# Performance work log

Hardware: AMD Instinct MI355X
Metric: run time of the kernel (lower is better)

Reference implementation:

```python
import jax, jax.numpy as jnp
import numpy as np

B, P, C = 2, 512, 21          # images, proposals/image, classes (incl background)
REG = 5                       # xc, yc, w, h, angle(deg)
DET = 100                     # detections_per_img
IMW, IMH = 1024, 800
SCORE_THRESH = 0.05
NMS_THR = 0.5
WEIGHTS = (10.0, 10.0, 5.0, 5.0, 3.0)
BBOX_XFORM_CLIP = float(np.log(1000.0 / 16.0))
MAXV = 8                      # max vertices of quad-quad intersection


def setup_inputs() -> dict:
    key = jax.random.key(0)
    k1, k2, k3 = jax.random.split(key, 3)
    class_logits = jax.random.normal(k1, (B * P, C), jnp.float32)
    box_regression = jax.random.normal(k2, (B * P, C * REG), jnp.float32)
    u = jax.random.uniform(k3, (B * P, 5), jnp.float32)
    rrects = jnp.stack([
        u[:, 0] * IMW,            # xc
        u[:, 1] * IMH,            # yc
        u[:, 2] * 200.0 + 16.0,   # w
        u[:, 3] * 200.0 + 16.0,   # h
        u[:, 4] * 360.0 - 180.0,  # angle in degrees
    ], axis=1)
    return {"class_logits": class_logits, "box_regression": box_regression, "rrects": rrects}


def rect_pts(r):
    # r [..., 5] -> corner points [..., 4, 2] (CCW quad in math coords)
    xc, yc, w, h, ang = (r[..., i] for i in range(5))
    t = ang * (jnp.pi / 180.0)
    c, s = jnp.cos(t), jnp.sin(t)
    dx, dy = w * 0.5, h * 0.5
    ox = jnp.stack([-dx, dx, dx, -dx], -1)
    oy = jnp.stack([-dy, -dy, dy, dy], -1)
    x = xc[..., None] + c[..., None] * ox - s[..., None] * oy
    y = yc[..., None] + s[..., None] * ox + c[..., None] * oy
    return jnp.stack([x, y], -1)


def decode(deltas, anchors):
    # BoxCoder.decode for rotated boxes, weights (wx,wy,ww,wh,wa)
    d = deltas.reshape(-1, C, REG) / jnp.asarray(WEIGHTS, deltas.dtype)
    dx, dy, dw, dh, da = (d[..., i] for i in range(REG))
    dw = jnp.minimum(dw, BBOX_XFORM_CLIP)
    dh = jnp.minimum(dh, BBOX_XFORM_CLIP)
    xc, yc, w, h, a = (anchors[:, i:i + 1] for i in range(5))
    px = dx * w + xc
    py = dy * h + yc
    pw = jnp.exp(dw) * w
    ph = jnp.exp(dh) * h
    pa = da * (180.0 / jnp.pi) + a
    return jnp.stack([px, py, pw, ph, pa], -1)  # [N, C, 5]


def _clip_edge(poly, n, a, b):
    # Sutherland-Hodgman clip of convex poly (buffer [MAXV,2], count n) by halfplane left of a->b
    d = b - a
    out = jnp.zeros((MAXV, 2), poly.dtype)
    m = jnp.int32(0)
    nn = jnp.maximum(n, 1)
    for i in range(MAXV):
        act = i < n
        s = poly[i]
        e = poly[jnp.mod(i + 1, nn)]
        cs = d[0] * (s[1] - a[1]) - d[1] * (s[0] - a[0])
        ce = d[0] * (e[1] - a[1]) - d[1] * (e[0] - a[0])
        denom = cs - ce
        t = cs / jnp.where(jnp.abs(denom) > 1e-12, denom, 1e-12)
        ip = s + t * (e - s)
        s_in = cs >= 0
        e_in = ce >= 0
        app1 = act & (s_in != e_in)           # crossing -> intersection point
        out = out.at[m].set(jnp.where(app1, ip, out[m]))
        m = m + app1.astype(jnp.int32)
        app2 = act & e_in                     # end point inside -> keep it
        out = out.at[m].set(jnp.where(app2, e, out[m]))
        m = m + app2.astype(jnp.int32)
    return out, m


def inter_area(p1, p2):
    # exact intersection area of two convex quads [4,2]
    poly = jnp.zeros((MAXV, 2), p1.dtype).at[:4].set(p1)
    n = jnp.int32(4)
    for k in range(4):
        poly, n = _clip_edge(poly, n, p2[k], p2[(k + 1) % 4])
    idx = jnp.arange(MAXV)
    nn = jnp.maximum(n, 1)
    nxt = jnp.mod(idx + 1, nn)
    cross = poly[:, 0] * poly[nxt, 1] - poly[nxt, 0] * poly[:, 1]
    area = 0.5 * jnp.abs(jnp.sum(jnp.where(idx < n, cross, 0.0)))
    return jnp.where(n >= 3, area, 0.0)


def _nms_one(args):
    # greedy rotated NMS on one (image,class) score-sorted set
    rr, valid = args                       # [P,5], [P] bool (sorted by desc score)
    pts = rect_pts(rr)                     # [P,4,2]
    areas = rr[:, 2] * rr[:, 3]
    inter = jax.vmap(lambda p: jax.vmap(lambda q: inter_area(p, q))(pts))(pts)
    iou = inter / (areas[:, None] + areas[None, :] - inter + 1e-8)
    n = rr.shape[0]
    def body(i, keep):
        sup = jnp.any(keep & (iou[i] > NMS_THR))
        return keep.at[i].set(valid[i] & jnp.logical_not(sup))
    return jax.lax.fori_loop(0, n, body, jnp.zeros((n,), bool))


def reference(class_logits, box_regression, rrects):
    scores = jax.nn.softmax(class_logits, -1)           # [N,C]
    proposals = decode(box_regression, rrects)          # [N,C,5]
    pts = rect_pts(proposals)                           # [N,C,4,2]
    mn, mx = pts.min(-2), pts.max(-2)
    bb = jnp.concatenate([mn, mx], -1)                  # xyxy [N,C,4]
    bb = jnp.stack([
        jnp.clip(bb[..., 0], 0.0, IMW - 1.0),
        jnp.clip(bb[..., 1], 0.0, IMH - 1.0),
        jnp.clip(bb[..., 2], 0.0, IMW - 1.0),
        jnp.clip(bb[..., 3], 0.0, IMH - 1.0),
    ], -1)

    # per-image, foreground classes only; [B, C-1, P, ...]
    sc = scores.reshape(B, P, C)[:, :, 1:].transpose(0, 2, 1)
    pr = proposals.reshape(B, P, C, 5)[:, :, 1:].transpose(0, 2, 1, 3)
    bx = bb.reshape(B, P, C, 4)[:, :, 1:].transpose(0, 2, 1, 3)

    valid = sc > SCORE_THRESH
    masked = jnp.where(valid, sc, -1.0)
    order = jnp.argsort(-masked, axis=-1)               # desc score per class
    sc_s = jnp.take_along_axis(masked, order, -1)
    valid_s = jnp.take_along_axis(valid, order, -1)
    pr_s = jnp.take_along_axis(pr, order[..., None], 2)
    bx_s = jnp.take_along_axis(bx, order[..., None], 2)

    keep = jax.lax.map(_nms_one, (jax.lax.stop_gradient(pr_s).reshape(-1, P, 5),
                                  valid_s.reshape(-1, P))).reshape(B, C - 1, P)
    keep = jax.lax.stop_gradient(keep)

    msk = jnp.where(keep, sc_s, -1.0)
    flat_s = msk.reshape(B, -1)                         # [B,(C-1)*P]
    top_idx = jax.lax.top_k(flat_s, DET)[1]
    sel_s = jnp.take_along_axis(flat_s, top_idx, -1)
    ok = sel_s > 0.0
    sel_bb = jnp.take_along_axis(bx_s.reshape(B, -1, 4), top_idx[..., None], 1)
    sel_rr = jnp.take_along_axis(pr_s.reshape(B, -1, 5), top_idx[..., None], 1)
    lab = jnp.broadcast_to(jnp.arange(1, C, dtype=jnp.int32)[:, None], (C - 1, P)).reshape(-1)
    sel_lab = lab[top_idx]

    out_bb = jnp.where(ok[..., None], sel_bb, 0.0)
    out_rr = jnp.where(ok[..., None], sel_rr, 0.0)
    out_sc = jnp.where(ok, sel_s, 0.0)
    out_lab = jnp.where(ok, sel_lab, 0)
    return out_bb, out_rr, out_sc, out_lab
```

## Files before the change

kernel.cpp:

```cpp
#include <hip/hip_runtime.h>
#include <stdint.h>

#pragma clang fp contract(off)

#define B_ 2
#define P_ 512
#define C_ 21
#define CF 20
#define DET 100
#define SCORE_THRESH 0.05f
#define NMS_THR 0.5f
#define BBOX_CLIP 4.135166556742356f
#define NC (CF * DET)

typedef unsigned long long u64;
typedef unsigned int u32;

__device__ __forceinline__ u32 f2o(float f) {
  u32 u = __float_as_uint(f);
  return (u & 0x80000000u) ? ~u : (u | 0x80000000u);
}
__device__ __forceinline__ float o2f(u32 o) {
  u32 u = (o & 0x80000000u) ? (o ^ 0x80000000u) : ~o;
  return __uint_as_float(u);
}

__global__ void __launch_bounds__(256)
prep_kernel(const float* __restrict__ logits,
            const float* __restrict__ breg,
            const float* __restrict__ rrects,
            float* __restrict__ scsS,
            float* __restrict__ ptsS,
            float* __restrict__ aabbS,
            float* __restrict__ pr5S,
            float* __restrict__ areaS,
            int* __restrict__ gV,
            u64* __restrict__ sup) {
  int g = blockIdx.x;
  int b = g / CF, cf = g % CF, c = cf + 1;
  int tid = threadIdx.x;

  __shared__ u64 lkey[P_];
  __shared__ int cnt;
  if (tid == 0) cnt = 0;

  u64 kreg[2];
  float fx[2][4], fy[2][4];
  float fab[2][4];
  float fp5[2][5];
  float far_[2];
  float fsc[2];
  #pragma unroll
  for (int e = 0; e < 2; ++e) {
    int p = tid + e * 256;
    int n = b * P_ + p;
    const float* lg = logits + n * C_;
    float mx = lg[0];
    for (int k = 1; k < C_; ++k) mx = fmaxf(mx, lg[k]);
    float den = 0.f;
    for (int k = 0; k < C_; ++k) den += expf(lg[k] - mx);
    float sc = expf(lg[c] - mx) / den;

    const float* d = breg + n * (C_ * 5) + c * 5;
    float dx = d[0] / 10.0f, dy = d[1] / 10.0f;
    float dw = d[2] / 5.0f, dh = d[3] / 5.0f, da = d[4] / 3.0f;
    dw = fminf(dw, BBOX_CLIP);
    dh = fminf(dh, BBOX_CLIP);
    const float* an = rrects + n * 5;
    float px = dx * an[2] + an[0];
    float py = dy * an[3] + an[1];
    float pw = expf(dw) * an[2];
    float ph = expf(dh) * an[3];
    float pa = da * 57.29577951308232f + an[4];
    fp5[e][0] = px; fp5[e][1] = py; fp5[e][2] = pw; fp5[e][3] = ph; fp5[e][4] = pa;
    far_[e] = pw * ph;

    float t = pa * 0.017453292519943295f;
    float cs = cosf(t), sn = sinf(t);
    float hx = pw * 0.5f, hy = ph * 0.5f;
    float ox[4] = {-hx, hx, hx, -hx};
    float oy[4] = {-hy, -hy, hy, hy};
    float minx = 1e30f, miny = 1e30f, maxx = -1e30f, maxy = -1e30f;
    #pragma unroll
    for (int qq = 0; qq < 4; ++qq) {
      float x = px + cs * ox[qq] - sn * oy[qq];
      float y = py + sn * ox[qq] + cs * oy[qq];
      fx[e][qq] = x; fy[e][qq] = y;
      minx = fminf(minx, x); maxx = fmaxf(maxx, x);
      miny = fminf(miny, y); maxy = fmaxf(maxy, y);
    }
    fab[e][0] = minx; fab[e][1] = miny; fab[e][2] = maxx; fab[e][3] = maxy;

    bool valid = sc > SCORE_THRESH;
    float v = valid ? sc : -1.0f;
    fsc[e] = v;
    u64 key = ((u64)f2o(v) << 32) | (u32)(~(u32)p);
    lkey[p] = key;
    kreg[e] = key;
    u64 m = __ballot(valid);
    if ((tid & 63) == 0) atomicAdd(&cnt, __popcll(m));
  }
  for (int w = tid; w < P_ * 8; w += 256) sup[(size_t)g * P_ * 8 + w] = 0ull;
  __syncthreads();

  u64 k0 = kreg[0], k1 = kreg[1];
  int r0 = 0, r1 = 0;
  for (int s = 0; s < P_; ++s) {
    u64 ks = lkey[s];
    r0 += (ks > k0) ? 1 : 0;
    r1 += (ks > k1) ? 1 : 0;
  }
  #pragma unroll
  for (int e = 0; e < 2; ++e) {
    if (fsc[e] > 0.f) {
      int r = (e == 0) ? r0 : r1;
      int so = g * P_ + r;
      scsS[so] = fsc[e];
      ((float4*)ptsS)[so * 2]     = make_float4(fx[e][0], fx[e][1], fx[e][2], fx[e][3]);
      ((float4*)ptsS)[so * 2 + 1] = make_float4(fy[e][0], fy[e][1], fy[e][2], fy[e][3]);
      ((float4*)aabbS)[so] = make_float4(fab[e][0], fab[e][1], fab[e][2], fab[e][3]);
      pr5S[so * 5 + 0] = fp5[e][0]; pr5S[so * 5 + 1] = fp5[e][1];
      pr5S[so * 5 + 2] = fp5[e][2]; pr5S[so * 5 + 3] = fp5[e][3];
      pr5S[so * 5 + 4] = fp5[e][4];
      areaS[so] = far_[e];
    }
  }
  if (tid == 0) gV[g] = cnt;
}

__device__ __forceinline__ float inter_area_reg(const float qx[4], const float qy[4],
                                                const float rx[4], const float ry[4]) {
  float px_[8], py_[8];
  #pragma unroll
  for (int t = 0; t < 8; ++t) { px_[t] = (t < 4) ? qx[t] : 0.f; py_[t] = (t < 4) ? qy[t] : 0.f; }
  int n = 4;
  #pragma unroll
  for (int e = 0; e < 4; ++e) {
    float a0 = rx[e], a1 = ry[e];
    float b0 = rx[(e + 1) & 3], b1 = ry[(e + 1) & 3];
    float dx = b0 - a0, dy = b1 - a1;
    float ox_[8], oy_[8];
    #pragma unroll
    for (int t = 0; t < 8; ++t) { ox_[t] = 0.f; oy_[t] = 0.f; }
    float cr[8];
    #pragma unroll
    for (int t = 0; t < 8; ++t) cr[t] = dx * (py_[t] - a1) - dy * (px_[t] - a0);
    int m = 0;
    int nn = (n > 1) ? n : 1;
    #pragma unroll
    for (int t = 0; t < 8; ++t) {
      bool act = t < n;
      float sx = px_[t], sy = py_[t];
      float ex, ey, ce;
      if (t == 7) { ex = px_[0]; ey = py_[0]; ce = cr[0]; }
      else {
        bool wrap = (t + 1 == nn);
        ex = wrap ? px_[0] : px_[t + 1];
        ey = wrap ? py_[0] : py_[t + 1];
        ce = wrap ? cr[0] : cr[t + 1];
      }
      float cs = cr[t];
      float denom = cs - ce;
      float dn = (fabsf(denom) > 1e-12f) ? denom : 1e-12f;
      float tt = cs / dn;
      float ipx = sx + tt * (ex - sx);
      float ipy = sy + tt * (ey - sy);
      bool s_in = cs >= 0.f, e_in = ce >= 0.f;
      bool app1 = act && (s_in != e_in);
      #pragma unroll
      for (int s2 = 0; s2 < 8; ++s2) {
        bool wr = app1 && (m == s2);
        ox_[s2] = wr ? ipx : ox_[s2];
        oy_[s2] = wr ? ipy : oy_[s2];
      }
      m += app1 ? 1 : 0;
      bool app2 = act && e_in;
      #pragma unroll
      for (int s2 = 0; s2 < 8; ++s2) {
        bool wr = app2 && (m == s2);
        ox_[s2] = wr ? ex : ox_[s2];
        oy_[s2] = wr ? ey : oy_[s2];
      }
      m += app2 ? 1 : 0;
    }
    n = m;
    #pragma unroll
    for (int t = 0; t < 8; ++t) { px_[t] = ox_[t]; py_[t] = oy_[t]; }
  }
  int nn = (n > 1) ? n : 1;
  float s = 0.f;
  #pragma unroll
  for (int t = 0; t < 8; ++t) {
    if (t < n) {
      float nx_x, nx_y;
      if (t == 7) { nx_x = px_[0]; nx_y = py_[0]; }
      else {
        bool wrap = (t + 1 == nn);
        nx_x = wrap ? px_[0] : px_[t + 1];
        nx_y = wrap ? py_[0] : py_[t + 1];
      }
      s += px_[t] * nx_y - nx_x * py_[t];
    }
  }
  float area = 0.5f * fabsf(s);
  return (n >= 3) ? area : 0.f;
}

#define PPT 4
#define TPB 256
__global__ void pair_kernel(const int* __restrict__ gV,
                            const float* __restrict__ aabbS,
                            const float* __restrict__ areaS,
                            const float* __restrict__ ptsS,
                            u64* __restrict__ sup) {
  int g = blockIdx.y;
  int V = gV[g];
  int Tp = V * (V - 1) / 2;
  int base = blockIdx.x * (TPB * PPT);
  if (base >= Tp) return;
  __shared__ u32 q[TPB * PPT];
  __shared__ int qn;
  int tid = threadIdx.x;
  if (tid == 0) qn = 0;
  __syncthreads();
  const float4* ab = (const float4*)aabbS;
  for (int t = 0; t < PPT; ++t) {
    int kk = base + t * TPB + tid;
    if (kk >= Tp) break;
    float kf = (float)kk;
    int i = (int)((1.0f + sqrtf(1.0f + 8.0f * kf)) * 0.5f);
    while (i * (i - 1) / 2 > kk) --i;
    while ((i + 1) * i / 2 <= kk) ++i;
    int j = kk - i * (i - 1) / 2;
    float4 bi = ab[g * P_ + i];
    float4 bj = ab[g * P_ + j];
    bool ov = (bi.x <= bj.z) && (bj.x <= bi.z) && (bi.y <= bj.w) && (bj.y <= bi.w);
    if (ov) {
      int s = atomicAdd(&qn, 1);
      q[s] = (u32)((i << 9) | j);
    }
  }
  __syncthreads();
  int nq = qn;
  const float4* pS = (const float4*)ptsS;
  for (int s = tid; s < nq; s += TPB) {
    u32 pk = q[s];
    int i = (int)(pk >> 9), j = (int)(pk & 511);
    float4 ax = pS[(g * P_ + i) * 2];
    float4 ay = pS[(g * P_ + i) * 2 + 1];
    float4 bx = pS[(g * P_ + j) * 2];
    float4 by = pS[(g * P_ + j) * 2 + 1];
    float qx[4] = {ax.x, ax.y, ax.z, ax.w};
    float qy[4] = {ay.x, ay.y, ay.z, ay.w};
    float rx[4] = {bx.x, bx.y, bx.z, bx.w};
    float ry[4] = {by.x, by.y, by.z, by.w};
    float ai = areaS[g * P_ + i];
    float aj = areaS[g * P_ + j];
    float inter = inter_area_reg(qx, qy, rx, ry);
    float iou = inter / (((ai + aj) - inter) + 1e-8f);
    if (iou > NMS_THR)
      atomicOr(&sup[((size_t)g * P_ + i) * 8 + (j >> 6)], 1ull << (j & 63));
  }
}

__global__ void greedy_kernel(const float* __restrict__ scsS, const int* __restrict__ gV,
                              const float* __restrict__ aabbS, const float* __restrict__ pr5S,
                              const u64* __restrict__ sup,
                              u64* __restrict__ cand, float* __restrict__ rec) {
  int g = blockIdx.x;
  int tid = threadIdx.x;
  __shared__ u64 lsup[P_ * 8];
  __shared__ u32 skeep[16];
  int V = gV[g];
  for (int w = tid; w < V * 8; w += 64) lsup[w] = sup[(size_t)g * P_ * 8 + w];
  __syncthreads();
  u64 keepw = 0;
  u64 cur = (tid < 8 && V > 0) ? lsup[tid] : 0ull;
  for (int i = 0; i < V; ++i) {
    u64 nxt = (tid < 8 && (i + 1) < V) ? lsup[(i + 1) * 8 + tid] : 0ull;
    bool supd = __any((cur & keepw) != 0ull);
    if (!supd && tid == (i >> 6)) keepw |= 1ull << (i & 63);
    cur = nxt;
  }
  if (tid < 8) { skeep[tid * 2] = (u32)keepw; skeep[tid * 2 + 1] = (u32)(keepw >> 32); }
  __syncthreads();
  int cls = g % CF;
  int tot = 0;
  #pragma unroll
  for (int t = 0; t < 16; ++t) tot += __popc(skeep[t]);
  for (int r = tid; r < V; r += 64) {
    if ((skeep[r >> 5] >> (r & 31)) & 1u) {
      int slot = __popc(skeep[r >> 5] & ((1u << (r & 31)) - 1u));
      for (int t = 0; t < (r >> 5); ++t) slot += __popc(skeep[t]);
      if (slot < DET) {
        float sv = scsS[g * P_ + r];
        int flat = cls * P_ + r;
        cand[g * DET + slot] = ((u64)f2o(sv) << 32) | (u32)(~(u32)flat);
        int so = g * P_ + r;
        float* rr = rec + (size_t)(g * DET + slot) * 12;
        rr[0] = fminf(fmaxf(aabbS[so * 4 + 0], 0.f), 1023.0f);
        rr[1] = fminf(fmaxf(aabbS[so * 4 + 1], 0.f), 799.0f);
        rr[2] = fminf(fmaxf(aabbS[so * 4 + 2], 0.f), 1023.0f);
        rr[3] = fminf(fmaxf(aabbS[so * 4 + 3], 0.f), 799.0f);
        rr[4] = pr5S[so * 5 + 0]; rr[5] = pr5S[so * 5 + 1]; rr[6] = pr5S[so * 5 + 2];
        rr[7] = pr5S[so * 5 + 3]; rr[8] = pr5S[so * 5 + 4];
        rr[9] = sv;
        rr[10] = (float)(cls + 1);
        rr[11] = 0.f;
      }
    }
  }
  int fill = tot < DET ? tot : DET;
  for (int s = fill + tid; s < DET; s += 64) cand[g * DET + s] = 0ull;
}

__global__ void rank_kernel(const u64* __restrict__ cand, const float* __restrict__ rec,
                            float* __restrict__ out) {
  int b = blockIdx.y;
  int tid = threadIdx.x;
  __shared__ u64 lc[NC];
  __shared__ int ncand;
  if (tid == 0) ncand = 0;
  __syncthreads();
  int nz = 0;
  for (int i = tid; i < NC; i += 256) {
    u64 v = cand[b * NC + i];
    lc[i] = v;
    nz += (v != 0ull) ? 1 : 0;
  }
  u64 m = __ballot(nz > 0);
  if (nz > 0) atomicAdd(&ncand, nz);
  (void)m;
  __syncthreads();
  int ci = blockIdx.x * 256 + tid;
  if (ci >= NC) return;
  if (blockIdx.x == 0 && tid < DET && tid >= ncand) {
    int o_bb = (b * DET + tid) * 4;
    int o_rr = B_ * DET * 4 + (b * DET + tid) * 5;
    int o_sc = B_ * DET * 9 + b * DET + tid;
    int o_lab = B_ * DET * 10 + b * DET + tid;
    out[o_bb + 0] = 0.f; out[o_bb + 1] = 0.f; out[o_bb + 2] = 0.f; out[o_bb + 3] = 0.f;
    out[o_rr + 0] = 0.f; out[o_rr + 1] = 0.f; out[o_rr + 2] = 0.f;
    out[o_rr + 3] = 0.f; out[o_rr + 4] = 0.f;
    out[o_sc] = 0.f;
    out[o_lab] = 0.f;
  }
  u64 k = lc[ci];
  if (k == 0ull) return;
  int rank = 0;
  #pragma unroll
  for (int gp = 0; gp < CF; ++gp) {
    int lo = 0, hi = DET;
    while (lo < hi) {
      int mid = (lo + hi) >> 1;
      if (lc[gp * DET + mid] > k) lo = mid + 1; else hi = mid;
    }
    rank += lo;
  }
  if (rank >= DET) return;
  const float* rr = rec + (size_t)(b * NC + ci) * 12;
  int o_bb = (b * DET + rank) * 4;
  int o_rr = B_ * DET * 4 + (b * DET + rank) * 5;
  int o_sc = B_ * DET * 9 + b * DET + rank;
  int o_lab = B_ * DET * 10 + b * DET + rank;
  out[o_bb + 0] = rr[0]; out[o_bb + 1] = rr[1];
  out[o_bb + 2] = rr[2]; out[o_bb + 3] = rr[3];
  out[o_rr + 0] = rr[4]; out[o_rr + 1] = rr[5]; out[o_rr + 2] = rr[6];
  out[o_rr + 3] = rr[7]; out[o_rr + 4] = rr[8];
  out[o_sc] = rr[9];
  out[o_lab] = rr[10];
}

extern "C" void kernel_launch(void* const* d_in, const int* in_sizes, int n_in,
                              void* d_out, int out_size, void* d_ws, size_t ws_size,
                              hipStream_t stream) {
  const float* logits = (const float*)d_in[0];
  const float* breg   = (const float*)d_in[1];
  const float* rrects = (const float*)d_in[2];
  float* out = (float*)d_out;

  const int G = B_ * CF;
  u64*   sup  = (u64*)d_ws;
  u64*   cand = sup + (size_t)G * P_ * 8;
  int*   gV   = (int*)(cand + G * DET);
  float* scsS = (float*)(gV + 64);
  float* ptsS = scsS + (size_t)G * P_;
  float* aabbS = ptsS + (size_t)G * P_ * 8;
  float* pr5S = aabbS + (size_t)G * P_ * 4;
  float* areaS = pr5S + (size_t)G * P_ * 5;
  float* rec  = areaS + (size_t)G * P_;

  prep_kernel<<<G, 256, 0, stream>>>(logits, breg, rrects,
                                     scsS, ptsS, aabbS, pr5S, areaS, gV, sup);
  pair_kernel<<<dim3(128, G), TPB, 0, stream>>>(gV, aabbS, areaS, ptsS, sup);
  greedy_kernel<<<G, 64, 0, stream>>>(scsS, gV, aabbS, pr5S, sup, cand, rec);
  rank_kernel<<<dim3((NC + 255) / 256, B_), 256, 0, stream>>>(cand, rec, out);
}
```

Baseline: 133.4 us.

## Fuse pair, greedy and rank kernels via last-block-done atomic counters

Merges the pairwise IoU, greedy NMS and cross-class ranking kernels into one launch. Completion counters in global memory let the last pair block of each group run the greedy step, and the last group of each image run the ranking. This removes two kernel launches and their gaps, at the cost of running the greedy and rank stages on a single block each, with serialized tail work and extra fences and atomics.

```diff
diff --git a/kernel.cpp b/kernel.cpp
--- a/kernel.cpp
+++ b/kernel.cpp
@@ -7,11 +7,15 @@
 #define P_ 512
 #define C_ 21
 #define CF 20
+#define G_ (B_ * CF)
 #define DET 100
 #define SCORE_THRESH 0.05f
 #define NMS_THR 0.5f
 #define BBOX_CLIP 4.135166556742356f
 #define NC (CF * DET)
+#define PPT 4
+#define TPB 256
+#define NBLK 128
 
 typedef unsigned long long u64;
 typedef unsigned int u32;
@@ -19,10 +23,6 @@
 __device__ __forceinline__ u32 f2o(float f) {
   u32 u = __float_as_uint(f);
   return (u & 0x80000000u) ? ~u : (u | 0x80000000u);
-}
-__device__ __forceinline__ float o2f(u32 o) {
-  u32 u = (o & 0x80000000u) ? (o ^ 0x80000000u) : ~o;
-  return __uint_as_float(u);
 }
 
 __global__ void __launch_bounds__(256)
@@ -35,21 +35,23 @@
             float* __restrict__ pr5S,
             float* __restrict__ areaS,
             int* __restrict__ gV,
-            u64* __restrict__ sup) {
+            u64* __restrict__ sup,
+            int* __restrict__ pairCnt,
+            int* __restrict__ grpCnt) {
   int g = blockIdx.x;
   int b = g / CF, cf = g % CF, c = cf + 1;
   int tid = threadIdx.x;
 
   __shared__ u64 lkey[P_];
   __shared__ int cnt;
-  if (tid == 0) cnt = 0;
+  if (tid == 0) {
+    cnt = 0;
+    pairCnt[g] = 0;
+    if (g < B_) grpCnt[g] = 0;
+  }
 
   u64 kreg[2];
-  float fx[2][4], fy[2][4];
-  float fab[2][4];
-  float fp5[2][5];
-  float far_[2];
-  float fsc[2];
+  float fx[2][4], fy[2][4], fab[2][4], fp5[2][5], far_[2], fsc[2];
   #pragma unroll
   for (int e = 0; e < 2; ++e) {
     int p = tid + e * 256;
@@ -206,169 +208,189 @@
   return (n >= 3) ? area : 0.f;
 }
 
-#define PPT 4
-#define TPB 256
-__global__ void pair_kernel(const int* __restrict__ gV,
-                            const float* __restrict__ aabbS,
-                            const float* __restrict__ areaS,
-                            const float* __restrict__ ptsS,
-                            u64* __restrict__ sup) {
+__global__ void __launch_bounds__(256)
+mega_kernel(const int* __restrict__ gV,
+            const float* __restrict__ aabbS,
+            const float* __restrict__ areaS,
+            const float* __restrict__ ptsS,
+            const float* __restrict__ scsS,
+            const float* __restrict__ pr5S,
+            u64* __restrict__ sup,
+            u64* __restrict__ cand,
+            float* __restrict__ rec,
+            float* __restrict__ out,
+            int* __restrict__ pairCnt,
+            int* __restrict__ grpCnt) {
   int g = blockIdx.y;
-  int V = gV[g];
-  int Tp = V * (V - 1) / 2;
-  int base = blockIdx.x * (TPB * PPT);
-  if (base >= Tp) return;
-  __shared__ u32 q[TPB * PPT];
-  __shared__ int qn;
   int tid = threadIdx.x;
-  if (tid == 0) qn = 0;
+  __shared__ u64 shbuf[P_ * 8];
+  __shared__ int scnt;
+  __shared__ int amLast;
+
+  {
+    int V = gV[g];
+    int Tp = V * (V - 1) / 2;
+    int base = blockIdx.x * (TPB * PPT);
+    if (base < Tp) {
+      u32* q = (u32*)shbuf;
+      if (tid == 0) scnt = 0;
+      __syncthreads();
+      const float4* ab = (const float4*)aabbS;
+      #pragma unroll
+      for (int t = 0; t < PPT; ++t) {
+        int kk = base + t * TPB + tid;
+        if (kk >= Tp) break;
+        float kf = (float)kk;
+        int i = (int)((1.0f + sqrtf(1.0f + 8.0f * kf)) * 0.5f);
+        while (i * (i - 1) / 2 > kk) --i;
+        while ((i + 1) * i / 2 <= kk) ++i;
+        int j = kk - i * (i - 1) / 2;
+        float4 bi = ab[g * P_ + i];
+        float4 bj = ab[g * P_ + j];
+        bool ov = (bi.x <= bj.z) && (bj.x <= bi.z) && (bi.y <= bj.w) && (bj.y <= bi.w);
+        if (ov) {
+          int s = atomicAdd(&scnt, 1);
+          q[s] = (u32)((i << 9) | j);
+        }
+      }
+      __syncthreads();
+      int nq = scnt;
+      const float4* pS = (const float4*)ptsS;
+      for (int s = tid; s < nq; s += TPB) {
+        u32 pk = q[s];
+        int i = (int)(pk >> 9), j = (int)(pk & 511);
+        float4 ax = pS[(g * P_ + i) * 2];
+        float4 ay = pS[(g * P_ + i) * 2 + 1];
+        float4 bx = pS[(g * P_ + j) * 2];
+        float4 by = pS[(g * P_ + j) * 2 + 1];
+        float qx[4] = {ax.x, ax.y, ax.z, ax.w};
+        float qy[4] = {ay.x, ay.y, ay.z, ay.w};
+        float rx[4] = {bx.x, bx.y, bx.z, bx.w};
+        float ry[4] = {by.x, by.y, by.z, by.w};
+        float ai = areaS[g * P_ + i];
+        float aj = areaS[g * P_ + j];
+        float inter = inter_area_reg(qx, qy, rx, ry);
+        float iou = inter / (((ai + aj) - inter) + 1e-8f);
+        if (iou > NMS_THR)
+          atomicOr(&sup[((size_t)g * P_ + i) * 8 + (j >> 6)], 1ull << (j & 63));
+      }
+    }
+  }
+
   __syncthreads();
-  const float4* ab = (const float4*)aabbS;
-  for (int t = 0; t < PPT; ++t) {
-    int kk = base + t * TPB + tid;
-    if (kk >= Tp) break;
-    float kf = (float)kk;
-    int i = (int)((1.0f + sqrtf(1.0f + 8.0f * kf)) * 0.5f);
-    while (i * (i - 1) / 2 > kk) --i;
-    while ((i + 1) * i / 2 <= kk) ++i;
-    int j = kk - i * (i - 1) / 2;
-    float4 bi = ab[g * P_ + i];
-    float4 bj = ab[g * P_ + j];
-    bool ov = (bi.x <= bj.z) && (bj.x <= bi.z) && (bi.y <= bj.w) && (bj.y <= bi.w);
-    if (ov) {
-      int s = atomicAdd(&qn, 1);
-      q[s] = (u32)((i << 9) | j);
-    }
-  }
+  __threadfence();
+  if (tid == 0) amLast = (atomicAdd(&pairCnt[g], 1) == NBLK - 1) ? 1 : 0;
   __syncthreads();
-  int nq = qn;
-  const float4* pS = (const float4*)ptsS;
-  for (int s = tid; s < nq; s += TPB) {
-    u32 pk = q[s];
-    int i = (int)(pk >> 9), j = (int)(pk & 511);
-    float4 ax = pS[(g * P_ + i) * 2];
-    float4 ay = pS[(g * P_ + i) * 2 + 1];
-    float4 bx = pS[(g * P_ + j) * 2];
-    float4 by = pS[(g * P_ + j) * 2 + 1];
-    float qx[4] = {ax.x, ax.y, ax.z, ax.w};
-    float qy[4] = {ay.x, ay.y, ay.z, ay.w};
-    float rx[4] = {bx.x, bx.y, bx.z, bx.w};
-    float ry[4] = {by.x, by.y, by.z, by.w};
-    float ai = areaS[g * P_ + i];
-    float aj = areaS[g * P_ + j];
-    float inter = inter_area_reg(qx, qy, rx, ry);
-    float iou = inter / (((ai + aj) - inter) + 1e-8f);
-    if (iou > NMS_THR)
-      atomicOr(&sup[((size_t)g * P_ + i) * 8 + (j >> 6)], 1ull << (j & 63));
-  }
-}
-
-__global__ void greedy_kernel(const float* __restrict__ scsS, const int* __restrict__ gV,
-                              const float* __restrict__ aabbS, const float* __restrict__ pr5S,
-                              const u64* __restrict__ sup,
-                              u64* __restrict__ cand, float* __restrict__ rec) {
-  int g = blockIdx.x;
-  int tid = threadIdx.x;
-  __shared__ u64 lsup[P_ * 8];
-  __shared__ u32 skeep[16];
-  int V = gV[g];
-  for (int w = tid; w < V * 8; w += 64) lsup[w] = sup[(size_t)g * P_ * 8 + w];
+  if (!amLast) return;
+  __threadfence();
+
+  {
+    u64* lsup = shbuf;
+    __shared__ u32 skeep[16];
+    int V = gV[g];
+    for (int w = tid; w < V * 8; w += TPB) lsup[w] = sup[(size_t)g * P_ * 8 + w];
+    __syncthreads();
+    if (tid < 64) {
+      u64 keepw = 0;
+      u64 cur = (tid < 8 && V > 0) ? lsup[tid] : 0ull;
+      for (int i = 0; i < V; ++i) {
+        u64 nxt = (tid < 8 && (i + 1) < V) ? lsup[(i + 1) * 8 + tid] : 0ull;
+        bool supd = __any((cur & keepw) != 0ull);
+        if (!supd && tid == (i >> 6)) keepw |= 1ull << (i & 63);
+        cur = nxt;
+      }
+      if (tid < 8) { skeep[tid * 2] = (u32)keepw; skeep[tid * 2 + 1] = (u32)(keepw >> 32); }
+    }
+    __syncthreads();
+    int cls = g % CF;
+    int tot = 0;
+    #pragma unroll
+    for (int t = 0; t < 16; ++t) tot += __popc(skeep[t]);
+    for (int r = tid; r < V; r += TPB) {
+      if ((skeep[r >> 5] >> (r & 31)) & 1u) {
+        int slot = __popc(skeep[r >> 5] & ((1u << (r & 31)) - 1u));
+        for (int t = 0; t < (r >> 5); ++t) slot += __popc(skeep[t]);
+        if (slot < DET) {
+          float sv = scsS[g * P_ + r];
+          int flat = cls * P_ + r;
+          cand[g * DET + slot] = ((u64)f2o(sv) << 32) | (u32)(~(u32)flat);
+          int so = g * P_ + r;
+          float* rr = rec + (size_t)(g * DET + slot) * 12;
+          rr[0] = fminf(fmaxf(aabbS[so * 4 + 0], 0.f), 1023.0f);
+          rr[1] = fminf(fmaxf(aabbS[so * 4 + 1], 0.f), 799.0f);
+          rr[2] = fminf(fmaxf(aabbS[so * 4 + 2], 0.f), 1023.0f);
+          rr[3] = fminf(fmaxf(aabbS[so * 4 + 3], 0.f), 799.0f);
+          rr[4] = pr5S[so * 5 + 0]; rr[5] = pr5S[so * 5 + 1]; rr[6] = pr5S[so * 5 + 2];
+          rr[7] = pr5S[so * 5 + 3]; rr[8] = pr5S[so * 5 + 4];
+          rr[9] = sv;
+          rr[10] = (float)(cls + 1);
+          rr[11] = 0.f;
+        }
+      }
+    }
+    int fill = tot < DET ? tot : DET;
+    for (int s = fill + tid; s < DET; s += TPB) cand[g * DET + s] = 0ull;
+  }
+
   __syncthreads();
-  u64 keepw = 0;
-  u64 cur = (tid < 8 && V > 0) ? lsup[tid] : 0ull;
-  for (int i = 0; i < V; ++i) {
-    u64 nxt = (tid < 8 && (i + 1) < V) ? lsup[(i + 1) * 8 + tid] : 0ull;
-    bool supd = __any((cur & keepw) != 0ull);
-    if (!supd && tid == (i >> 6)) keepw |= 1ull << (i & 63);
-    cur = nxt;
-  }
-  if (tid < 8) { skeep[tid * 2] = (u32)keepw; skeep[tid * 2 + 1] = (u32)(keepw >> 32); }
+  __threadfence();
+  int b = g / CF;
+  if (tid == 0) amLast = (atomicAdd(&grpCnt[b], 1) == CF - 1) ? 1 : 0;
   __syncthreads();
-  int cls = g % CF;
-  int tot = 0;
-  #pragma unroll
-  for (int t = 0; t < 16; ++t) tot += __popc(skeep[t]);
-  for (int r = tid; r < V; r += 64) {
-    if ((skeep[r >> 5] >> (r & 31)) & 1u) {
-      int slot = __popc(skeep[r >> 5] & ((1u << (r & 31)) - 1u));
-      for (int t = 0; t < (r >> 5); ++t) slot += __popc(skeep[t]);
-      if (slot < DET) {
-        float sv = scsS[g * P_ + r];
-        int flat = cls * P_ + r;
-        cand[g * DET + slot] = ((u64)f2o(sv) << 32) | (u32)(~(u32)flat);
-        int so = g * P_ + r;
-        float* rr = rec + (size_t)(g * DET + slot) * 12;
-        rr[0] = fminf(fmaxf(aabbS[so * 4 + 0], 0.f), 1023.0f);
-        rr[1] = fminf(fmaxf(aabbS[so * 4 + 1], 0.f), 799.0f);
-        rr[2] = fminf(fmaxf(aabbS[so * 4 + 2], 0.f), 1023.0f);
-        rr[3] = fminf(fmaxf(aabbS[so * 4 + 3], 0.f), 799.0f);
-        rr[4] = pr5S[so * 5 + 0]; rr[5] = pr5S[so * 5 + 1]; rr[6] = pr5S[so * 5 + 2];
-        rr[7] = pr5S[so * 5 + 3]; rr[8] = pr5S[so * 5 + 4];
-        rr[9] = sv;
-        rr[10] = (float)(cls + 1);
-        rr[11] = 0.f;
-      }
-    }
-  }
-  int fill = tot < DET ? tot : DET;
-  for (int s = fill + tid; s < DET; s += 64) cand[g * DET + s] = 0ull;
-}
-
-__global__ void rank_kernel(const u64* __restrict__ cand, const float* __restrict__ rec,
-                            float* __restrict__ out) {
-  int b = blockIdx.y;
-  int tid = threadIdx.x;
-  __shared__ u64 lc[NC];
-  __shared__ int ncand;
-  if (tid == 0) ncand = 0;
-  __syncthreads();
-  int nz = 0;
-  for (int i = tid; i < NC; i += 256) {
-    u64 v = cand[b * NC + i];
-    lc[i] = v;
-    nz += (v != 0ull) ? 1 : 0;
-  }
-  u64 m = __ballot(nz > 0);
-  if (nz > 0) atomicAdd(&ncand, nz);
-  (void)m;
-  __syncthreads();
-  int ci = blockIdx.x * 256 + tid;
-  if (ci >= NC) return;
-  if (blockIdx.x == 0 && tid < DET && tid >= ncand) {
-    int o_bb = (b * DET + tid) * 4;
-    int o_rr = B_ * DET * 4 + (b * DET + tid) * 5;
-    int o_sc = B_ * DET * 9 + b * DET + tid;
-    int o_lab = B_ * DET * 10 + b * DET + tid;
-    out[o_bb + 0] = 0.f; out[o_bb + 1] = 0.f; out[o_bb + 2] = 0.f; out[o_bb + 3] = 0.f;
-    out[o_rr + 0] = 0.f; out[o_rr + 1] = 0.f; out[o_rr + 2] = 0.f;
-    out[o_rr + 3] = 0.f; out[o_rr + 4] = 0.f;
-    out[o_sc] = 0.f;
-    out[o_lab] = 0.f;
-  }
-  u64 k = lc[ci];
-  if (k == 0ull) return;
-  int rank = 0;
-  #pragma unroll
-  for (int gp = 0; gp < CF; ++gp) {
-    int lo = 0, hi = DET;
-    while (lo < hi) {
-      int mid = (lo + hi) >> 1;
-      if (lc[gp * DET + mid] > k) lo = mid + 1; else hi = mid;
-    }
-    rank += lo;
-  }
-  if (rank >= DET) return;
-  const float* rr = rec + (size_t)(b * NC + ci) * 12;
-  int o_bb = (b * DET + rank) * 4;
-  int o_rr = B_ * DET * 4 + (b * DET + rank) * 5;
-  int o_sc = B_ * DET * 9 + b * DET + rank;
-  int o_lab = B_ * DET * 10 + b * DET + rank;
-  out[o_bb + 0] = rr[0]; out[o_bb + 1] = rr[1];
-  out[o_bb + 2] = rr[2]; out[o_bb + 3] = rr[3];
-  out[o_rr + 0] = rr[4]; out[o_rr + 1] = rr[5]; out[o_rr + 2] = rr[6];
-  out[o_rr + 3] = rr[7]; out[o_rr + 4] = rr[8];
-  out[o_sc] = rr[9];
-  out[o_lab] = rr[10];
+  if (!amLast) return;
+  __threadfence();
+
+  {
+    u64* lc = shbuf;
+    if (tid == 0) scnt = 0;
+    __syncthreads();
+    int nz = 0;
+    for (int i = tid; i < NC; i += TPB) {
+      u64 v = cand[b * NC + i];
+      lc[i] = v;
+      nz += (v != 0ull) ? 1 : 0;
+    }
+    if (nz > 0) atomicAdd(&scnt, nz);
+    __syncthreads();
+    int nc = scnt;
+    for (int row = nc + tid; row < DET; row += TPB) {
+      int o_bb = (b * DET + row) * 4;
+      int o_rr = B_ * DET * 4 + (b * DET + row) * 5;
+      int o_sc = B_ * DET * 9 + b * DET + row;
+      int o_lab = B_ * DET * 10 + b * DET + row;
+      out[o_bb + 0] = 0.f; out[o_bb + 1] = 0.f; out[o_bb + 2] = 0.f; out[o_bb + 3] = 0.f;
+      out[o_rr + 0] = 0.f; out[o_rr + 1] = 0.f; out[o_rr + 2] = 0.f;
+      out[o_rr + 3] = 0.f; out[o_rr + 4] = 0.f;
+      out[o_sc] = 0.f;
+      out[o_lab] = 0.f;
+    }
+    for (int ci = tid; ci < NC; ci += TPB) {
+      u64 k = lc[ci];
+      if (k == 0ull) continue;
+      int rank = 0;
+      #pragma unroll
+      for (int gp = 0; gp < CF; ++gp) {
+        int lo = 0, hi = DET;
+        while (lo < hi) {
+          int mid = (lo + hi) >> 1;
+          if (lc[gp * DET + mid] > k) lo = mid + 1; else hi = mid;
+        }
+        rank += lo;
+      }
+      if (rank >= DET) continue;
+      const float* rr = rec + (size_t)(b * NC + ci) * 12;
+      int o_bb = (b * DET + rank) * 4;
+      int o_rr = B_ * DET * 4 + (b * DET + rank) * 5;
+      int o_sc = B_ * DET * 9 + b * DET + rank;
+      int o_lab = B_ * DET * 10 + b * DET + rank;
+      out[o_bb + 0] = rr[0]; out[o_bb + 1] = rr[1];
+      out[o_bb + 2] = rr[2]; out[o_bb + 3] = rr[3];
+      out[o_rr + 0] = rr[4]; out[o_rr + 1] = rr[5]; out[o_rr + 2] = rr[6];
+      out[o_rr + 3] = rr[7]; out[o_rr + 4] = rr[8];
+      out[o_sc] = rr[9];
+      out[o_lab] = rr[10];
+    }
+  }
 }
 
 extern "C" void kernel_launch(void* const* d_in, const int* in_sizes, int n_in,
@@ -379,20 +401,22 @@
   const float* rrects = (const float*)d_in[2];
   float* out = (float*)d_out;
 
-  const int G = B_ * CF;
-  u64*   sup  = (u64*)d_ws;
-  u64*   cand = sup + (size_t)G * P_ * 8;
-  int*   gV   = (int*)(cand + G * DET);
-  float* scsS = (float*)(gV + 64);
-  float* ptsS = scsS + (size_t)G * P_;
-  float* aabbS = ptsS + (size_t)G * P_ * 8;
-  float* pr5S = aabbS + (size_t)G * P_ * 4;
-  float* areaS = pr5S + (size_t)G * P_ * 5;
-  float* rec  = areaS + (size_t)G * P_;
-
-  prep_kernel<<<G, 256, 0, stream>>>(logits, breg, rrects,
-                                     scsS, ptsS, aabbS, pr5S, areaS, gV, sup);
-  pair_kernel<<<dim3(128, G), TPB, 0, stream>>>(gV, aabbS, areaS, ptsS, sup);
-  greedy_kernel<<<G, 64, 0, stream>>>(scsS, gV, aabbS, pr5S, sup, cand, rec);
-  rank_kernel<<<dim3((NC + 255) / 256, B_), 256, 0, stream>>>(cand, rec, out);
+  u64*   sup    = (u64*)d_ws;
+  u64*   cand   = sup + (size_t)G_ * P_ * 8;
+  int*   gV     = (int*)(cand + G_ * DET);
+  int*   pairCnt = gV + 64;
+  int*   grpCnt  = pairCnt + 64;
+  float* scsS   = (float*)(grpCnt + 16);
+  float* ptsS   = scsS + (size_t)G_ * P_;
+  float* aabbS  = ptsS + (size_t)G_ * P_ * 8;
+  float* pr5S   = aabbS + (size_t)G_ * P_ * 4;
+  float* areaS  = pr5S + (size_t)G_ * P_ * 5;
+  float* rec    = areaS + (size_t)G_ * P_;
+
+  prep_kernel<<<G_, 256, 0, stream>>>(logits, breg, rrects,
+                                      scsS, ptsS, aabbS, pr5S, areaS, gV, sup,
+                                      pairCnt, grpCnt);
+  mega_kernel<<<dim3(NBLK, G_), TPB, 0, stream>>>(gV, aabbS, areaS, ptsS,
+                                                  scsS, pr5S, sup, cand, rec,
+                                                  out, pairCnt, grpCnt);
 }
```

Result: slower. 475.8 us (+256.7%).

## Fuse decode into pair kernel with per-chunk suppression lists and LDS geometry

Applied to the files above, without the earlier changes.

Merges the prep and pair kernels. Each of 32 blocks per class-group recomputes the decode, softmax and rank sort, then keeps the sorted corners, AABBs and areas in LDS for the pairwise IoU tests. Suppressing pairs are written as per-chunk compact lists instead of atomically OR-ing into a global bitmask that had to be zeroed first. The greedy kernel rebuilds the bitmask in LDS from these lists with 256 threads. This removes one launch, the global corner/area buffers and the zeroing pass, at the cost of doing the decode redundantly in every block.

```diff
diff --git a/kernel.cpp b/kernel.cpp
--- a/kernel.cpp
+++ b/kernel.cpp
@@ -7,11 +7,16 @@
 #define P_ 512
 #define C_ 21
 #define CF 20
+#define G_ (B_ * CF)
 #define DET 100
 #define SCORE_THRESH 0.05f
 #define NMS_THR 0.5f
 #define BBOX_CLIP 4.135166556742356f
 #define NC (CF * DET)
+#define TPB 256
+#define NBX 32
+#define CHUNK 1024
+#define MAXCH 128
 
 typedef unsigned long long u64;
 typedef unsigned int u32;
@@ -20,36 +25,111 @@
   u32 u = __float_as_uint(f);
   return (u & 0x80000000u) ? ~u : (u | 0x80000000u);
 }
-__device__ __forceinline__ float o2f(u32 o) {
-  u32 u = (o & 0x80000000u) ? (o ^ 0x80000000u) : ~o;
-  return __uint_as_float(u);
+
+__device__ __forceinline__ float inter_area_reg(const float qx[4], const float qy[4],
+                                                const float rx[4], const float ry[4]) {
+  float px_[8], py_[8];
+  #pragma unroll
+  for (int t = 0; t < 8; ++t) { px_[t] = (t < 4) ? qx[t] : 0.f; py_[t] = (t < 4) ? qy[t] : 0.f; }
+  int n = 4;
+  #pragma unroll
+  for (int e = 0; e < 4; ++e) {
+    float a0 = rx[e], a1 = ry[e];
+    float b0 = rx[(e + 1) & 3], b1 = ry[(e + 1) & 3];
+    float dx = b0 - a0, dy = b1 - a1;
+    float ox_[8], oy_[8];
+    #pragma unroll
+    for (int t = 0; t < 8; ++t) { ox_[t] = 0.f; oy_[t] = 0.f; }
+    float cr[8];
+    #pragma unroll
+    for (int t = 0; t < 8; ++t) cr[t] = dx * (py_[t] - a1) - dy * (px_[t] - a0);
+    int m = 0;
+    int nn = (n > 1) ? n : 1;
+    #pragma unroll
+    for (int t = 0; t < 8; ++t) {
+      bool act = t < n;
+      float sx = px_[t], sy = py_[t];
+      float ex, ey, ce;
+      if (t == 7) { ex = px_[0]; ey = py_[0]; ce = cr[0]; }
+      else {
+        bool wrap = (t + 1 == nn);
+        ex = wrap ? px_[0] : px_[t + 1];
+        ey = wrap ? py_[0] : py_[t + 1];
+        ce = wrap ? cr[0] : cr[t + 1];
+      }
+      float cs = cr[t];
+      float denom = cs - ce;
+      float dn = (fabsf(denom) > 1e-12f) ? denom : 1e-12f;
+      float tt = cs / dn;
+      float ipx = sx + tt * (ex - sx);
+      float ipy = sy + tt * (ey - sy);
+      bool s_in = cs >= 0.f, e_in = ce >= 0.f;
+      bool app1 = act && (s_in != e_in);
+      #pragma unroll
+      for (int s2 = 0; s2 < 8; ++s2) {
+        bool wr = app1 && (m == s2);
+        ox_[s2] = wr ? ipx : ox_[s2];
+        oy_[s2] = wr ? ipy : oy_[s2];
+      }
+      m += app1 ? 1 : 0;
+      bool app2 = act && e_in;
+      #pragma unroll
+      for (int s2 = 0; s2 < 8; ++s2) {
+        bool wr = app2 && (m == s2);
+        ox_[s2] = wr ? ex : ox_[s2];
+        oy_[s2] = wr ? ey : oy_[s2];
+      }
+      m += app2 ? 1 : 0;
+    }
+    n = m;
+    #pragma unroll
+    for (int t = 0; t < 8; ++t) { px_[t] = ox_[t]; py_[t] = oy_[t]; }
+  }
+  int nn = (n > 1) ? n : 1;
+  float s = 0.f;
+  #pragma unroll
+  for (int t = 0; t < 8; ++t) {
+    if (t < n) {
+      float nx_x, nx_y;
+      if (t == 7) { nx_x = px_[0]; nx_y = py_[0]; }
+      else {
+        bool wrap = (t + 1 == nn);
+        nx_x = wrap ? px_[0] : px_[t + 1];
+        nx_y = wrap ? py_[0] : py_[t + 1];
+      }
+      s += px_[t] * nx_y - nx_x * py_[t];
+    }
+  }
+  float area = 0.5f * fabsf(s);
+  return (n >= 3) ? area : 0.f;
 }
 
 __global__ void __launch_bounds__(256)
-prep_kernel(const float* __restrict__ logits,
-            const float* __restrict__ breg,
-            const float* __restrict__ rrects,
-            float* __restrict__ scsS,
-            float* __restrict__ ptsS,
-            float* __restrict__ aabbS,
-            float* __restrict__ pr5S,
-            float* __restrict__ areaS,
-            int* __restrict__ gV,
-            u64* __restrict__ sup) {
-  int g = blockIdx.x;
+pairdec_kernel(const float* __restrict__ logits,
+               const float* __restrict__ breg,
+               const float* __restrict__ rrects,
+               u32* __restrict__ nsup,
+               u32* __restrict__ list,
+               int* __restrict__ gV,
+               float* __restrict__ scsS,
+               float* __restrict__ aabbS,
+               float* __restrict__ pr5S) {
+  int g = blockIdx.y;
+  int bx = blockIdx.x;
+  int tid = threadIdx.x;
   int b = g / CF, cf = g % CF, c = cf + 1;
-  int tid = threadIdx.x;
 
   __shared__ u64 lkey[P_];
-  __shared__ int cnt;
-  if (tid == 0) cnt = 0;
+  __shared__ float lptx[4][P_];
+  __shared__ float lpty[4][P_];
+  __shared__ float lab4[4][P_];
+  __shared__ float larea[P_];
+  __shared__ u32 q[CHUNK];
+  __shared__ int qn, sn, sV;
+  if (tid == 0) sV = 0;
 
   u64 kreg[2];
-  float fx[2][4], fy[2][4];
-  float fab[2][4];
-  float fp5[2][5];
-  float far_[2];
-  float fsc[2];
+  float fx[2][4], fy[2][4], fab[2][4], fp5[2][5], far_[2], fsc[2];
   #pragma unroll
   for (int e = 0; e < 2; ++e) {
     int p = tid + e * 256;
@@ -76,15 +156,15 @@
     far_[e] = pw * ph;
 
     float t = pa * 0.017453292519943295f;
-    float cs = cosf(t), sn = sinf(t);
+    float cs = cosf(t), sn2 = sinf(t);
     float hx = pw * 0.5f, hy = ph * 0.5f;
     float ox[4] = {-hx, hx, hx, -hx};
     float oy[4] = {-hy, -hy, hy, hy};
     float minx = 1e30f, miny = 1e30f, maxx = -1e30f, maxy = -1e30f;
     #pragma unroll
     for (int qq = 0; qq < 4; ++qq) {
-      float x = px + cs * ox[qq] - sn * oy[qq];
-      float y = py + sn * ox[qq] + cs * oy[qq];
+      float x = px + cs * ox[qq] - sn2 * oy[qq];
+      float y = py + sn2 * ox[qq] + cs * oy[qq];
       fx[e][qq] = x; fy[e][qq] = y;
       minx = fminf(minx, x); maxx = fmaxf(maxx, x);
       miny = fminf(miny, y); maxy = fmaxf(maxy, y);
@@ -98,9 +178,8 @@
     lkey[p] = key;
     kreg[e] = key;
     u64 m = __ballot(valid);
-    if ((tid & 63) == 0) atomicAdd(&cnt, __popcll(m));
-  }
-  for (int w = tid; w < P_ * 8; w += 256) sup[(size_t)g * P_ * 8 + w] = 0ull;
+    if ((tid & 63) == 0) atomicAdd(&sV, __popcll(m));
+  }
   __syncthreads();
 
   u64 k0 = kreg[0], k1 = kreg[1];
@@ -112,183 +191,120 @@
   }
   #pragma unroll
   for (int e = 0; e < 2; ++e) {
-    if (fsc[e] > 0.f) {
-      int r = (e == 0) ? r0 : r1;
+    int r = (e == 0) ? r0 : r1;
+    #pragma unroll
+    for (int qq = 0; qq < 4; ++qq) {
+      lptx[qq][r] = fx[e][qq];
+      lpty[qq][r] = fy[e][qq];
+      lab4[qq][r] = fab[e][qq];
+    }
+    larea[r] = far_[e];
+    if (bx == 0) {
       int so = g * P_ + r;
       scsS[so] = fsc[e];
-      ((float4*)ptsS)[so * 2]     = make_float4(fx[e][0], fx[e][1], fx[e][2], fx[e][3]);
-      ((float4*)ptsS)[so * 2 + 1] = make_float4(fy[e][0], fy[e][1], fy[e][2], fy[e][3]);
       ((float4*)aabbS)[so] = make_float4(fab[e][0], fab[e][1], fab[e][2], fab[e][3]);
       pr5S[so * 5 + 0] = fp5[e][0]; pr5S[so * 5 + 1] = fp5[e][1];
       pr5S[so * 5 + 2] = fp5[e][2]; pr5S[so * 5 + 3] = fp5[e][3];
       pr5S[so * 5 + 4] = fp5[e][4];
-      areaS[so] = far_[e];
-    }
-  }
-  if (tid == 0) gV[g] = cnt;
-}
-
-__device__ __forceinline__ float inter_area_reg(const float qx[4], const float qy[4],
-                                                const float rx[4], const float ry[4]) {
-  float px_[8], py_[8];
-  #pragma unroll
-  for (int t = 0; t < 8; ++t) { px_[t] = (t < 4) ? qx[t] : 0.f; py_[t] = (t < 4) ? qy[t] : 0.f; }
-  int n = 4;
-  #pragma unroll
-  for (int e = 0; e < 4; ++e) {
-    float a0 = rx[e], a1 = ry[e];
-    float b0 = rx[(e + 1) & 3], b1 = ry[(e + 1) & 3];
-    float dx = b0 - a0, dy = b1 - a1;
-    float ox_[8], oy_[8];
-    #pragma unroll
-    for (int t = 0; t < 8; ++t) { ox_[t] = 0.f; oy_[t] = 0.f; }
-    float cr[8];
-    #pragma unroll
-    for (int t = 0; t < 8; ++t) cr[t] = dx * (py_[t] - a1) - dy * (px_[t] - a0);
-    int m = 0;
-    int nn = (n > 1) ? n : 1;
-    #pragma unroll
-    for (int t = 0; t < 8; ++t) {
-      bool act = t < n;
-      float sx = px_[t], sy = py_[t];
-      float ex, ey, ce;
-      if (t == 7) { ex = px_[0]; ey = py_[0]; ce = cr[0]; }
-      else {
-        bool wrap = (t + 1 == nn);
-        ex = wrap ? px_[0] : px_[t + 1];
-        ey = wrap ? py_[0] : py_[t + 1];
-        ce = wrap ? cr[0] : cr[t + 1];
-      }
-      float cs = cr[t];
-      float denom = cs - ce;
-      float dn = (fabsf(denom) > 1e-12f) ? denom : 1e-12f;
-      float tt = cs / dn;
-      float ipx = sx + tt * (ex - sx);
-      float ipy = sy + tt * (ey - sy);
-      bool s_in = cs >= 0.f, e_in = ce >= 0.f;
-      bool app1 = act && (s_in != e_in);
-      #pragma unroll
-      for (int s2 = 0; s2 < 8; ++s2) {
-        bool wr = app1 && (m == s2);
-        ox_[s2] = wr ? ipx : ox_[s2];
-        oy_[s2] = wr ? ipy : oy_[s2];
-      }
-      m += app1 ? 1 : 0;
-      bool app2 = act && e_in;
-      #pragma unroll
-      for (int s2 = 0; s2 < 8; ++s2) {
-        bool wr = app2 && (m == s2);
-        ox_[s2] = wr ? ex : ox_[s2];
-        oy_[s2] = wr ? ey : oy_[s2];
-      }
-      m += app2 ? 1 : 0;
-    }
-    n = m;
-    #pragma unroll
-    for (int t = 0; t < 8; ++t) { px_[t] = ox_[t]; py_[t] = oy_[t]; }
-  }
-  int nn = (n > 1) ? n : 1;
-  float s = 0.f;
-  #pragma unroll
-  for (int t = 0; t < 8; ++t) {
-    if (t < n) {
-      float nx_x, nx_y;
-      if (t == 7) { nx_x = px_[0]; nx_y = py_[0]; }
-      else {
-        bool wrap = (t + 1 == nn);
-        nx_x = wrap ? px_[0] : px_[t + 1];
-        nx_y = wrap ? py_[0] : py_[t + 1];
-      }
-      s += px_[t] * nx_y - nx_x * py_[t];
-    }
-  }
-  float area = 0.5f * fabsf(s);
-  return (n >= 3) ? area : 0.f;
-}
-
-#define PPT 4
-#define TPB 256
-__global__ void pair_kernel(const int* __restrict__ gV,
-                            const float* __restrict__ aabbS,
-                            const float* __restrict__ areaS,
-                            const float* __restrict__ ptsS,
-                            u64* __restrict__ sup) {
-  int g = blockIdx.y;
-  int V = gV[g];
+    }
+  }
+  __syncthreads();
+  int V = sV;
+  if (bx == 0 && tid == 0) gV[g] = V;
   int Tp = V * (V - 1) / 2;
-  int base = blockIdx.x * (TPB * PPT);
-  if (base >= Tp) return;
-  __shared__ u32 q[TPB * PPT];
-  __shared__ int qn;
-  int tid = threadIdx.x;
-  if (tid == 0) qn = 0;
-  __syncthreads();
-  const float4* ab = (const float4*)aabbS;
-  for (int t = 0; t < PPT; ++t) {
-    int kk = base + t * TPB + tid;
-    if (kk >= Tp) break;
-    float kf = (float)kk;
-    int i = (int)((1.0f + sqrtf(1.0f + 8.0f * kf)) * 0.5f);
-    while (i * (i - 1) / 2 > kk) --i;
-    while ((i + 1) * i / 2 <= kk) ++i;
-    int j = kk - i * (i - 1) / 2;
-    float4 bi = ab[g * P_ + i];
-    float4 bj = ab[g * P_ + j];
-    bool ov = (bi.x <= bj.z) && (bj.x <= bi.z) && (bi.y <= bj.w) && (bj.y <= bi.w);
-    if (ov) {
-      int s = atomicAdd(&qn, 1);
-      q[s] = (u32)((i << 9) | j);
-    }
-  }
-  __syncthreads();
-  int nq = qn;
-  const float4* pS = (const float4*)ptsS;
-  for (int s = tid; s < nq; s += TPB) {
-    u32 pk = q[s];
-    int i = (int)(pk >> 9), j = (int)(pk & 511);
-    float4 ax = pS[(g * P_ + i) * 2];
-    float4 ay = pS[(g * P_ + i) * 2 + 1];
-    float4 bx = pS[(g * P_ + j) * 2];
-    float4 by = pS[(g * P_ + j) * 2 + 1];
-    float qx[4] = {ax.x, ax.y, ax.z, ax.w};
-    float qy[4] = {ay.x, ay.y, ay.z, ay.w};
-    float rx[4] = {bx.x, bx.y, bx.z, bx.w};
-    float ry[4] = {by.x, by.y, by.z, by.w};
-    float ai = areaS[g * P_ + i];
-    float aj = areaS[g * P_ + j];
-    float inter = inter_area_reg(qx, qy, rx, ry);
-    float iou = inter / (((ai + aj) - inter) + 1e-8f);
-    if (iou > NMS_THR)
-      atomicOr(&sup[((size_t)g * P_ + i) * 8 + (j >> 6)], 1ull << (j & 63));
-  }
-}
-
-__global__ void greedy_kernel(const float* __restrict__ scsS, const int* __restrict__ gV,
-                              const float* __restrict__ aabbS, const float* __restrict__ pr5S,
-                              const u64* __restrict__ sup,
-                              u64* __restrict__ cand, float* __restrict__ rec) {
+
+  for (int ch = bx; ch < MAXCH; ch += NBX)
+    if (tid == 0) nsup[g * MAXCH + ch] = 0;
+
+  for (int ch = bx; ch * CHUNK < Tp; ch += NBX) {
+    int base = ch * CHUNK;
+    if (tid == 0) { qn = 0; sn = 0; }
+    __syncthreads();
+    #pragma unroll
+    for (int t = 0; t < 4; ++t) {
+      int kk = base + t * TPB + tid;
+      if (kk >= Tp) break;
+      float kf = (float)kk;
+      int i = (int)((1.0f + sqrtf(1.0f + 8.0f * kf)) * 0.5f);
+      while (i * (i - 1) / 2 > kk) --i;
+      while ((i + 1) * i / 2 <= kk) ++i;
+      int j = kk - i * (i - 1) / 2;
+      bool ov = (lab4[0][i] <= lab4[2][j]) && (lab4[0][j] <= lab4[2][i]) &&
+                (lab4[1][i] <= lab4[3][j]) && (lab4[1][j] <= lab4[3][i]);
+      if (ov) {
+        int s = atomicAdd(&qn, 1);
+        q[s] = (u32)((i << 9) | j);
+      }
+    }
+    __syncthreads();
+    int nq = qn;
+    u32* Lout = list + ((size_t)g * MAXCH + ch) * CHUNK;
+    for (int s = tid; s < nq; s += TPB) {
+      u32 pk = q[s];
+      int i = (int)(pk >> 9), j = (int)(pk & 511);
+      float qx[4] = {lptx[0][i], lptx[1][i], lptx[2][i], lptx[3][i]};
+      float qy[4] = {lpty[0][i], lpty[1][i], lpty[2][i], lpty[3][i]};
+      float rx[4] = {lptx[0][j], lptx[1][j], lptx[2][j], lptx[3][j]};
+      float ry[4] = {lpty[0][j], lpty[1][j], lpty[2][j], lpty[3][j]};
+      float ai = larea[i];
+      float aj = larea[j];
+      float inter = inter_area_reg(qx, qy, rx, ry);
+      float iou = inter / (((ai + aj) - inter) + 1e-8f);
+      if (iou > NMS_THR) {
+        int idx = atomicAdd(&sn, 1);
+        Lout[idx] = pk;
+      }
+    }
+    __syncthreads();
+    if (tid == 0) nsup[g * MAXCH + ch] = (u32)sn;
+  }
+}
+
+__global__ void __launch_bounds__(256)
+greedy_kernel(const u32* __restrict__ nsup, const u32* __restrict__ list,
+              const int* __restrict__ gV, const float* __restrict__ scsS,
+              const float* __restrict__ aabbS, const float* __restrict__ pr5S,
+              u64* __restrict__ cand, float* __restrict__ rec) {
   int g = blockIdx.x;
   int tid = threadIdx.x;
-  __shared__ u64 lsup[P_ * 8];
+  __shared__ u32 supb[P_][16];
+  __shared__ u32 lnsup[MAXCH];
   __shared__ u32 skeep[16];
   int V = gV[g];
-  for (int w = tid; w < V * 8; w += 64) lsup[w] = sup[(size_t)g * P_ * 8 + w];
-  __syncthreads();
-  u64 keepw = 0;
-  u64 cur = (tid < 8 && V > 0) ? lsup[tid] : 0ull;
-  for (int i = 0; i < V; ++i) {
-    u64 nxt = (tid < 8 && (i + 1) < V) ? lsup[(i + 1) * 8 + tid] : 0ull;
-    bool supd = __any((cur & keepw) != 0ull);
-    if (!supd && tid == (i >> 6)) keepw |= 1ull << (i & 63);
-    cur = nxt;
-  }
-  if (tid < 8) { skeep[tid * 2] = (u32)keepw; skeep[tid * 2 + 1] = (u32)(keepw >> 32); }
-  __syncthreads();
+  for (int w = tid; w < P_ * 16; w += TPB) ((u32*)supb)[w] = 0u;
+  for (int i = tid; i < MAXCH; i += TPB) lnsup[i] = nsup[g * MAXCH + i];
+  __syncthreads();
+
+  for (int ch = 0; ch < MAXCH; ++ch) {
+    int n = (int)lnsup[ch];
+    if (n == 0) continue;
+    const u32* L = list + ((size_t)g * MAXCH + ch) * CHUNK;
+    for (int e = tid; e < n; e += TPB) {
+      u32 pk = L[e];
+      int i = (int)(pk >> 9), j = (int)(pk & 511);
+      atomicOr(&supb[i][j >> 5], 1u << (j & 31));
+    }
+  }
+  __syncthreads();
+
+  if (tid < 64) {
+    u32 keepw = 0;
+    u32 cur = (tid < 16 && V > 0) ? supb[0][tid] : 0u;
+    for (int i = 0; i < V; ++i) {
+      u32 nxt = (tid < 16 && (i + 1) < V) ? supb[i + 1][tid] : 0u;
+      bool supd = __any((cur & keepw) != 0u);
+      if (!supd && tid == (i >> 5)) keepw |= 1u << (i & 31);
+      cur = nxt;
+    }
+    if (tid < 16) skeep[tid] = keepw;
+  }
+  __syncthreads();
+
   int cls = g % CF;
   int tot = 0;
   #pragma unroll
   for (int t = 0; t < 16; ++t) tot += __popc(skeep[t]);
-  for (int r = tid; r < V; r += 64) {
+  for (int r = tid; r < V; r += TPB) {
     if ((skeep[r >> 5] >> (r & 31)) & 1u) {
       int slot = __popc(skeep[r >> 5] & ((1u << (r & 31)) - 1u));
       for (int t = 0; t < (r >> 5); ++t) slot += __popc(skeep[t]);
@@ -311,7 +327,7 @@
     }
   }
   int fill = tot < DET ? tot : DET;
-  for (int s = fill + tid; s < DET; s += 64) cand[g * DET + s] = 0ull;
+  for (int s = fill + tid; s < DET; s += TPB) cand[g * DET + s] = 0ull;
 }
 
 __global__ void rank_kernel(const u64* __restrict__ cand, const float* __restrict__ rec,
@@ -328,13 +344,12 @@
     lc[i] = v;
     nz += (v != 0ull) ? 1 : 0;
   }
-  u64 m = __ballot(nz > 0);
   if (nz > 0) atomicAdd(&ncand, nz);
-  (void)m;
   __syncthreads();
   int ci = blockIdx.x * 256 + tid;
   if (ci >= NC) return;
-  if (blockIdx.x == 0 && tid < DET && tid >= ncand) {
+  int nc = ncand;
+  if (blockIdx.x == 0 && tid < DET && tid >= nc) {
     int o_bb = (b * DET + tid) * 4;
     int o_rr = B_ * DET * 4 + (b * DET + tid) * 5;
     int o_sc = B_ * DET * 9 + b * DET + tid;
@@ -379,20 +394,19 @@
   const float* rrects = (const float*)d_in[2];
   float* out = (float*)d_out;
 
-  const int G = B_ * CF;
-  u64*   sup  = (u64*)d_ws;
-  u64*   cand = sup + (size_t)G * P_ * 8;
-  int*   gV   = (int*)(cand + G * DET);
-  float* scsS = (float*)(gV + 64);
-  float* ptsS = scsS + (size_t)G * P_;
-  float* aabbS = ptsS + (size_t)G * P_ * 8;
-  float* pr5S = aabbS + (size_t)G * P_ * 4;
-  float* areaS = pr5S + (size_t)G * P_ * 5;
-  float* rec  = areaS + (size_t)G * P_;
-
-  prep_kernel<<<G, 256, 0, stream>>>(logits, breg, rrects,
-                                     scsS, ptsS, aabbS, pr5S, areaS, gV, sup);
-  pair_kernel<<<dim3(128, G), TPB, 0, stream>>>(gV, aabbS, areaS, ptsS, sup);
-  greedy_kernel<<<G, 64, 0, stream>>>(scsS, gV, aabbS, pr5S, sup, cand, rec);
-  rank_kernel<<<dim3((NC + 255) / 256, B_), 256, 0, stream>>>(cand, rec, out);
-}
+  u32*   nsup  = (u32*)d_ws;
+  u32*   list  = nsup + (size_t)G_ * MAXCH;
+  u64*   cand  = (u64*)(list + (size_t)G_ * MAXCH * CHUNK);
+  int*   gV    = (int*)(cand + G_ * DET);
+  float* scsS  = (float*)(gV + 64);
+  float* aabbS = scsS + (size_t)G_ * P_;
+  float* pr5S  = aabbS + (size_t)G_ * P_ * 4;
+  float* rec   = pr5S + (size_t)G_ * P_ * 5;
+
+  pairdec_kernel<<<dim3(NBX, G_), TPB, 0, stream>>>(logits, breg, rrects,
+                                                    nsup, list, gV,
+                                                    scsS, aabbS, pr5S);
+  greedy_kernel<<<G_, TPB, 0, stream>>>(nsup, list, gV, scsS, aabbS, pr5S,
+                                        cand, rec);
+  rank_kernel<<<dim3(8, B_), 256, 0, stream>>>(cand, rec, out);
+}
```

Result: slower. 148.7 us (+11.5%).
